# Optimization experiments

Measured on AMD Instinct MI355X. Metric: run time of the kernel, lower is better.

The kernel has to match this reference:

```python
import jax, jax.numpy as jnp
import numpy as np

TOKENS, IN_F, OUT_F = 8192, 4096, 4096
INPUT_ZERO_POINT = 3  # Z_x, baked into shifted_q_bias at quantization time
QMIN, QMAX = -128, 127  # 8-bit signed range


def setup_inputs() -> dict:
    key = jax.random.key(0)
    k1, k2, k3, k4 = jax.random.split(key, 4)
    # int8-valued quantized activations and per-output-channel symmetric int8 weights
    q_x = jax.random.randint(k1, (TOKENS, IN_F), -128, 128, dtype=jnp.int32)
    q_weight = jax.random.randint(k2, (OUT_F, IN_F), -127, 128, dtype=jnp.int32)
    # per-output-channel weight scale (symmetric per-channel quantization)
    weight_scale = jax.random.uniform(k3, (OUT_F,), minval=1e-3, maxval=1e-2, dtype=jnp.float32)
    # int32 quantized bias; shifted by the input zero-point correction term:
    # shifted_q_bias = q_bias - Z_x * q_W.sum(dim=1)
    q_bias = jax.random.randint(k4, (OUT_F,), -(2 ** 15), 2 ** 15, dtype=jnp.int32)
    shifted_q_bias = q_bias - INPUT_ZERO_POINT * jnp.sum(q_weight, axis=1, dtype=jnp.int32)
    return {
        "q_x": q_x,
        "q_weight": q_weight,
        "shifted_q_bias": shifted_q_bias,
        "weight_scale": weight_scale,
        "input_scale": jnp.float32(0.02),
        "output_scale": jnp.float32(0.05),
        "output_zero_point": jnp.float32(-5.0),
    }


def reference(q_x, q_weight, shifted_q_bias, weight_scale, input_scale, output_scale, output_zero_point):
    # GPU path of get_matmul_quantized_output: float-cast int GEMM with fused bias
    acc = jnp.dot(q_x.astype(jnp.float32), q_weight.T.astype(jnp.float32))
    acc = acc + shifted_q_bias.astype(jnp.float32)  # [tokens, out]
    # per-output-channel requant scale: S_W * S_X / S_Y
    scale = weight_scale * input_scale / output_scale  # [out]
    y = scale * acc + output_zero_point
    return jnp.clip(jnp.round(y), QMIN, QMAX).astype(jnp.int8)
```

## Files before the change

kernel.cpp:

```cpp
#include <hip/hip_runtime.h>

#define TOKENS 8192
#define IN_F   4096
#define OUT_F  4096

#define BM 256
#define BN 256
#define BKB 128
#define NT (IN_F / BKB)
#define NI (NT / 2)

using int4v = __attribute__((ext_vector_type(4))) int;
typedef __attribute__((address_space(3))) char       lds_char_t;
typedef const __attribute__((address_space(1))) char glob_char_t;

__global__ void pack_i32_to_i8(const int* __restrict__ src, int* __restrict__ dst, int n4) {
    int stride = gridDim.x * blockDim.x;
    for (int i = blockIdx.x * blockDim.x + threadIdx.x; i < n4; i += stride) {
        int4v v = ((const int4v*)src)[i];
        dst[i] = (v.x & 0xff) | ((v.y & 0xff) << 8) | ((v.z & 0xff) << 16) | (v.w << 24);
    }
}

__global__ __launch_bounds__(512, 2) void qgemm_i8(
    const signed char* __restrict__ A,
    const signed char* __restrict__ Bw,
    const int*   __restrict__ bias,
    const float* __restrict__ wscale,
    const float* __restrict__ p_si, const float* __restrict__ p_so, const float* __restrict__ p_zp,
    int* __restrict__ C)
{
    constexpr int N = OUT_F, K = IN_F;
    constexpr int NBN = N / BN;

    __shared__ __align__(16) signed char smem[131072];

    int nwg = gridDim.x, bid = blockIdx.x, swz = bid;
    if ((nwg & 7) == 0) { int cpx = nwg >> 3; swz = (bid & 7) * cpx + (bid >> 3); }
    int bm = swz / NBN, bn = swz - bm * NBN;

    const int t = threadIdx.x, wid = t >> 6, l = t & 63;
    const int wr = wid >> 2, wc = wid & 3, lr = l & 15, lg = l >> 4;

    const int k0off = ((lg       ^ (lr & 7)) << 4);
    const int k1off = (((4 + lg) ^ (lr & 7)) << 4);
    const int arow = (wr * 128 + lr) * 128;
    const int brow = (wc * 64  + lr) * 128;

    const int srow = t >> 3;
    const int scol = (((t & 7) ^ ((t >> 3) & 7)) << 4);
    const signed char* gApl = A  + (size_t)(bm * BM + srow) * K + scol;
    const signed char* gBpl = Bw + (size_t)(bn * BN + srow) * K + scol;

#define STA(bufOff_, h_, tt_) do {                                                                 \
    __builtin_amdgcn_global_load_lds((glob_char_t*)(gApl + (size_t)((h_)*128      ) * K + (tt_)*BKB), \
        (lds_char_t*)smem + (bufOff_) + (h_)*16384 +        wid*1024, 16, 0, 0);                   \
    __builtin_amdgcn_global_load_lds((glob_char_t*)(gApl + (size_t)((h_)*128 + 64 ) * K + (tt_)*BKB), \
        (lds_char_t*)smem + (bufOff_) + (h_)*16384 + 8192 + wid*1024, 16, 0, 0);                   \
} while (0)
#define STB(bufOff_, h_, tt_) do {                                                                 \
    __builtin_amdgcn_global_load_lds((glob_char_t*)(gBpl + (size_t)((h_)*128      ) * K + (tt_)*BKB), \
        (lds_char_t*)smem + (bufOff_) + 32768 + (h_)*16384 +        wid*1024, 16, 0, 0);           \
    __builtin_amdgcn_global_load_lds((glob_char_t*)(gBpl + (size_t)((h_)*128 + 64 ) * K + (tt_)*BKB), \
        (lds_char_t*)smem + (bufOff_) + 32768 + (h_)*16384 + 8192 + wid*1024, 16, 0, 0);           \
} while (0)

#define LDA4(bufOff_, mb_) do { _Pragma("unroll") for (int mm = 0; mm < 4; ++mm) {                 \
    a[(mb_)+mm][0] = *(const int4v*)(smem + (bufOff_) + arow + ((mb_)+mm)*2048 + k0off);           \
    a[(mb_)+mm][1] = *(const int4v*)(smem + (bufOff_) + arow + ((mb_)+mm)*2048 + k1off); } } while (0)
#define LDB2(bufOff_, nb_) do { _Pragma("unroll") for (int nn = 0; nn < 2; ++nn) {                 \
    b[(nb_)+nn][0] = *(const int4v*)(smem + (bufOff_) + 32768 + brow + ((nb_)+nn)*2048 + k0off);   \
    b[(nb_)+nn][1] = *(const int4v*)(smem + (bufOff_) + 32768 + brow + ((nb_)+nn)*2048 + k1off); } } while (0)

#define MF(mb_, nb_) do { _Pragma("unroll") for (int kk = 0; kk < 2; ++kk)                         \
    _Pragma("unroll") for (int mm = 0; mm < 4; ++mm)                                               \
    _Pragma("unroll") for (int nn = 0; nn < 2; ++nn)                                               \
        acc[(mb_)+mm][(nb_)+nn] = __builtin_amdgcn_mfma_i32_16x16x64_i8(                           \
            a[(mb_)+mm][kk], b[(nb_)+nn][kk], acc[(mb_)+mm][(nb_)+nn], 0, 0, 0); } while (0)

#define SP1 __builtin_amdgcn_s_setprio(1)
#define SP0 __builtin_amdgcn_s_setprio(0)
#define BAR __builtin_amdgcn_s_barrier()
#define VM(n_) asm volatile("s_waitcnt vmcnt(" #n_ ")" ::: "memory")

    int4v acc[8][4] = {};
    int4v a[8][2], b[4][2];

    STA(0, 0, 0); STA(0, 1, 0); STB(0, 0, 0); STB(0, 1, 0);
    STA(65536, 0, 1); STA(65536, 1, 1);
    VM(4);
    BAR;
    LDB2(0, 0); LDA4(0, 0);

#define ITER_FULL(i_) do {                                                                         \
    const int t1 = 2*(i_)+1, t2 = 2*(i_)+2, t3 = 2*(i_)+3;                                         \
     STB(65536, 0, t1); LDA4(0, 4);                  SP1; MF(0, 0); SP0;        BAR;         \
     STB(65536, 1, t1); LDB2(0, 2);                  SP1; MF(4, 0); SP0;        BAR;         \
     STA(0, 0, t2);                                  SP1; MF(0, 2); SP0; VM(2); BAR;         \
     STA(0, 1, t2);     LDB2(65536, 0); LDA4(65536, 0); SP1; MF(4, 2); SP0;     BAR;         \
     STB(0, 0, t2);     LDA4(65536, 4);              SP1; MF(0, 0); SP0;        BAR;         \
     STB(0, 1, t2);     LDB2(65536, 2);              SP1; MF(4, 0); SP0;        BAR;         \
     STA(65536, 0, t3);                              SP1; MF(0, 2); SP0; VM(2); BAR;         \
     STA(65536, 1, t3); LDB2(0, 0); LDA4(0, 0);      SP1; MF(4, 2); SP0;        BAR;         \
} while (0)

#define ITER_TAIL() do {                                                                           \
     STB(65536, 0, 31); LDA4(0, 4);                  SP1; MF(0, 0); SP0;        BAR;         \
     STB(65536, 1, 31); LDB2(0, 2);                  SP1; MF(4, 0); SP0;        BAR;         \
                                                     SP1; MF(0, 2); SP0; VM(0); BAR;         \
     LDB2(65536, 0); LDA4(65536, 0);                 SP1; MF(4, 2); SP0;        BAR;         \
     LDA4(65536, 4);                                 SP1; MF(0, 0); SP0;        BAR;         \
     LDB2(65536, 2);                                 SP1; MF(4, 0); SP0;        BAR;         \
                                                     SP1; MF(0, 2); SP0;        BAR;         \
                                                     SP1; MF(4, 2); SP0;                     \
} while (0)

    for (int i = 0; i < NI - 1; ++i) ITER_FULL(i);
    ITER_TAIL();

#undef ITER_TAIL
#undef ITER_FULL
#undef VM
#undef BAR
#undef SP0
#undef SP1
#undef MF
#undef LDB2
#undef LDA4
#undef STB
#undef STA

    float si = p_si[0], so = p_so[0], z = p_zp[0];
    float rs = si / so;

    #pragma unroll
    for (int n = 0; n < 4; ++n) {
        int col = bn * BN + wc * 64 + n * 16 + lr;
        float sc = wscale[col] * rs;
        int   bs = bias[col];
        #pragma unroll
        for (int m = 0; m < 8; ++m) {
            int row = bm * BM + wr * 128 + m * 16 + lg * 4;
            #pragma unroll
            for (int r = 0; r < 4; ++r) {
                float y = sc * (float)(acc[m][n][r] + bs) + z;
                y = rintf(y);
                y = fminf(fmaxf(y, -128.0f), 127.0f);
                C[(size_t)(row + r) * N + col] = (int)y;
            }
        }
    }
}

__global__ void qgemm_naive(const int* __restrict__ qx, const int* __restrict__ qw,
                            const int* __restrict__ bias, const float* __restrict__ wscale,
                            const float* __restrict__ si, const float* __restrict__ so,
                            const float* __restrict__ zp, int* __restrict__ out) {
    int idx = blockIdx.x * blockDim.x + threadIdx.x;
    if (idx >= TOKENS * OUT_F) return;
    int row = idx / OUT_F, col = idx - row * OUT_F;
    const int4v* xa = (const int4v*)(qx + (size_t)row * IN_F);
    const int4v* wb = (const int4v*)(qw + (size_t)col * IN_F);
    int acc = 0;
    for (int k = 0; k < IN_F / 4; ++k) {
        int4v a = xa[k], b = wb[k];
        acc += a.x * b.x + a.y * b.y + a.z * b.z + a.w * b.w;
    }
    float y = wscale[col] * si[0] / so[0] * (float)(acc + bias[col]) + zp[0];
    y = fminf(fmaxf(rintf(y), -128.0f), 127.0f);
    out[idx] = (int)y;
}

extern "C" void kernel_launch(void* const* d_in, const int* in_sizes, int n_in,
                              void* d_out, int out_size, void* d_ws, size_t ws_size,
                              hipStream_t stream) {
    const int*   q_x    = (const int*)d_in[0];
    const int*   q_w    = (const int*)d_in[1];
    const int*   bias   = (const int*)d_in[2];
    const float* wscale = (const float*)d_in[3];
    const float* s_in   = (const float*)d_in[4];
    const float* s_out  = (const float*)d_in[5];
    const float* zp     = (const float*)d_in[6];
    int* out = (int*)d_out;

    const size_t needA = (size_t)TOKENS * IN_F;
    const size_t needB = (size_t)OUT_F * IN_F;

    if (ws_size >= needA + needB) {
        signed char* pA = (signed char*)d_ws;
        signed char* pB = pA + needA;
        pack_i32_to_i8<<<2048, 256, 0, stream>>>(q_x, (int*)pA, (int)(needA / 4));
        pack_i32_to_i8<<<1024, 256, 0, stream>>>(q_w, (int*)pB, (int)(needB / 4));
        int grid = (TOKENS / BM) * (OUT_F / BN);
        qgemm_i8<<<grid, 512, 0, stream>>>(pA, pB, bias, wscale, s_in, s_out, zp, out);
    } else {
        int total = TOKENS * OUT_F;
        qgemm_naive<<<(total + 255) / 256, 256, 0, stream>>>(q_x, q_w, bias, wscale, s_in, s_out, zp, out);
    }
}
```

Measured before the change: 181.6 us.

## Switch int8 GEMM to 32x32x32 MFMA with inline-asm LDS reads and restructured pipeline

Replaces the 16x16x64 int8 MFMA tiling with 32x32x32 MFMA fragments, so each wave holds a 4x2 grid of 16-element accumulators. LDS reads become inline-asm ds_read_b128 with immediate offsets from precomputed swizzled base pointers that toggle between the two buffers. The main loop is rescheduled into four half-tile phases with ping-pong register fragments, explicit lgkmcnt/vmcnt waits and sched barriers. The aim is fewer MFMA issues, fewer LDS reads per MAC and less address arithmetic. In exchange, waiting on vmcnt(0) at every stage may expose global-load latency, and the epilogue row mapping must match the 32x32 output layout.

New measurement: 199.6 us. 9.9% more time.

```diff
diff --git a/kernel.cpp b/kernel.cpp
--- a/kernel.cpp
+++ b/kernel.cpp
@@ -10,7 +10,8 @@
 #define NT (IN_F / BKB)
 #define NI (NT / 2)
 
-using int4v = __attribute__((ext_vector_type(4))) int;
+using int4v  = __attribute__((ext_vector_type(4)))  int;
+using int16v = __attribute__((ext_vector_type(16))) int;
 typedef __attribute__((address_space(3))) char       lds_char_t;
 typedef const __attribute__((address_space(1))) char glob_char_t;
 
@@ -40,12 +41,17 @@
     int bm = swz / NBN, bn = swz - bm * NBN;
 
     const int t = threadIdx.x, wid = t >> 6, l = t & 63;
-    const int wr = wid >> 2, wc = wid & 3, lr = l & 15, lg = l >> 4;
-
-    const int k0off = ((lg       ^ (lr & 7)) << 4);
-    const int k1off = (((4 + lg) ^ (lr & 7)) << 4);
-    const int arow = (wr * 128 + lr) * 128;
-    const int brow = (wc * 64  + lr) * 128;
+    const int wr = wid >> 2, wc = wid & 3;
+    const int l31 = l & 31, hi = l >> 5, l7 = l & 7;
+
+    const unsigned aB0 = (unsigned)(uintptr_t)((lds_char_t*)smem + (wr * 128 + l31) * 128);
+    const unsigned bB0 = (unsigned)(uintptr_t)((lds_char_t*)smem + 32768 + (wc * 64 + l31) * 128);
+    unsigned aB[4], bB[4];
+    #pragma unroll
+    for (int k = 0; k < 4; ++k) {
+        unsigned x = (unsigned)(((k * 2 + hi) ^ l7) << 4);
+        aB[k] = aB0 + x; bB[k] = bB0 + x;
+    }
 
     const int srow = t >> 3;
     const int scol = (((t & 7) ^ ((t >> 3) & 7)) << 4);
@@ -65,54 +71,69 @@
         (lds_char_t*)smem + (bufOff_) + 32768 + (h_)*16384 + 8192 + wid*1024, 16, 0, 0);           \
 } while (0)
 
-#define LDA4(bufOff_, mb_) do { _Pragma("unroll") for (int mm = 0; mm < 4; ++mm) {                 \
-    a[(mb_)+mm][0] = *(const int4v*)(smem + (bufOff_) + arow + ((mb_)+mm)*2048 + k0off);           \
-    a[(mb_)+mm][1] = *(const int4v*)(smem + (bufOff_) + arow + ((mb_)+mm)*2048 + k1off); } } while (0)
-#define LDB2(bufOff_, nb_) do { _Pragma("unroll") for (int nn = 0; nn < 2; ++nn) {                 \
-    b[(nb_)+nn][0] = *(const int4v*)(smem + (bufOff_) + 32768 + brow + ((nb_)+nn)*2048 + k0off);   \
-    b[(nb_)+nn][1] = *(const int4v*)(smem + (bufOff_) + 32768 + brow + ((nb_)+nn)*2048 + k1off); } } while (0)
-
-#define MF(mb_, nb_) do { _Pragma("unroll") for (int kk = 0; kk < 2; ++kk)                         \
-    _Pragma("unroll") for (int mm = 0; mm < 4; ++mm)                                               \
-    _Pragma("unroll") for (int nn = 0; nn < 2; ++nn)                                               \
-        acc[(mb_)+mm][(nb_)+nn] = __builtin_amdgcn_mfma_i32_16x16x64_i8(                           \
-            a[(mb_)+mm][kk], b[(nb_)+nn][kk], acc[(mb_)+mm][(nb_)+nn], 0, 0, 0); } while (0)
-
+#define DSR(dst_, base_, imm_) \
+    asm volatile("ds_read_b128 %0, %1 offset:" #imm_ : "=&v"(dst_) : "v"(base_))
+
+#define RDH(aF_, bF_, k0_, k1_) do {                                     \
+    DSR(aF_[0][0], aB[k0_], 0);     DSR(aF_[0][1], aB[k1_], 0);          \
+    DSR(aF_[1][0], aB[k0_], 4096);  DSR(aF_[1][1], aB[k1_], 4096);       \
+    DSR(aF_[2][0], aB[k0_], 8192);  DSR(aF_[2][1], aB[k1_], 8192);       \
+    DSR(aF_[3][0], aB[k0_], 12288); DSR(aF_[3][1], aB[k1_], 12288);      \
+    DSR(bF_[0][0], bB[k0_], 0);     DSR(bF_[0][1], bB[k1_], 0);          \
+    DSR(bF_[1][0], bB[k0_], 4096);  DSR(bF_[1][1], bB[k1_], 4096); } while (0)
+
+#define SLOTP() do { _Pragma("unroll") for (int k_ = 0; k_ < 4; ++k_) { aB[k_] += 65536u; bB[k_] += 65536u; } } while (0)
+#define SLOTM() do { _Pragma("unroll") for (int k_ = 0; k_ < 4; ++k_) { aB[k_] -= 65536u; bB[k_] -= 65536u; } } while (0)
+
+#define MF(aF_, bF_) do { _Pragma("unroll") for (int kk = 0; kk < 2; ++kk)                         \
+    _Pragma("unroll") for (int mi = 0; mi < 4; ++mi)                                               \
+    _Pragma("unroll") for (int ni = 0; ni < 2; ++ni)                                               \
+        acc[mi][ni] = __builtin_amdgcn_mfma_i32_32x32x32_i8(                                       \
+            aF_[mi][kk], bF_[ni][kk], acc[mi][ni], 0, 0, 0); } while (0)
+
+#define SCB __builtin_amdgcn_sched_barrier(0)
 #define SP1 __builtin_amdgcn_s_setprio(1)
 #define SP0 __builtin_amdgcn_s_setprio(0)
 #define BAR __builtin_amdgcn_s_barrier()
-#define VM(n_) asm volatile("s_waitcnt vmcnt(" #n_ ")" ::: "memory")
-
-    int4v acc[8][4] = {};
-    int4v a[8][2], b[4][2];
+#define VM0 asm volatile("s_waitcnt vmcnt(0)" ::: "memory")
+#define WK0 do { asm volatile("s_waitcnt lgkmcnt(0)" ::: "memory"); SCB; } while (0)
+
+    int16v acc[4][2] = {};
+    int4v aE[4][2], aO[4][2], bE[2][2], bO[2][2];
 
     STA(0, 0, 0); STA(0, 1, 0); STB(0, 0, 0); STB(0, 1, 0);
     STA(65536, 0, 1); STA(65536, 1, 1);
-    VM(4);
+    VM0;
     BAR;
-    LDB2(0, 0); LDA4(0, 0);
+    RDH(aE, bE, 0, 1);
+    WK0;
 
 #define ITER_FULL(i_) do {                                                                         \
-    const int t1 = 2*(i_)+1, t2 = 2*(i_)+2, t3 = 2*(i_)+3;                                         \
-     STB(65536, 0, t1); LDA4(0, 4);                  SP1; MF(0, 0); SP0;        BAR;         \
-     STB(65536, 1, t1); LDB2(0, 2);                  SP1; MF(4, 0); SP0;        BAR;         \
-     STA(0, 0, t2);                                  SP1; MF(0, 2); SP0; VM(2); BAR;         \
-     STA(0, 1, t2);     LDB2(65536, 0); LDA4(65536, 0); SP1; MF(4, 2); SP0;     BAR;         \
-     STB(0, 0, t2);     LDA4(65536, 4);              SP1; MF(0, 0); SP0;        BAR;         \
-     STB(0, 1, t2);     LDB2(65536, 2);              SP1; MF(4, 0); SP0;        BAR;         \
-     STA(65536, 0, t3);                              SP1; MF(0, 2); SP0; VM(2); BAR;         \
-     STA(65536, 1, t3); LDB2(0, 0); LDA4(0, 0);      SP1; MF(4, 2); SP0;        BAR;         \
+    const int u1 = 2*(i_) + 1, u2 = 2*(i_) + 2, u3 = 2*(i_) + 3;                                   \
+                     \
+    STB(65536, 0, u1); STB(65536, 1, u1);                                                          \
+    RDH(aO, bO, 2, 3); SCB; SP1; MF(aE, bE); SP0; SCB; WK0; VM0; SLOTP(); BAR;                     \
+                 \
+    STA(0, 0, u2); STA(0, 1, u2);                                                                  \
+    RDH(aE, bE, 0, 1); SCB; SP1; MF(aO, bO); SP0; SCB; WK0; BAR;                                   \
+             \
+    STB(0, 0, u2); STB(0, 1, u2);                                                                  \
+    RDH(aO, bO, 2, 3); SCB; SP1; MF(aE, bE); SP0; SCB; WK0; VM0; SLOTM(); BAR;                     \
+                       \
+    STA(65536, 0, u3); STA(65536, 1, u3);                                                          \
+    RDH(aE, bE, 0, 1); SCB; SP1; MF(aO, bO); SP0; SCB; WK0; BAR;                                   \
 } while (0)
 
 #define ITER_TAIL() do {                                                                           \
-     STB(65536, 0, 31); LDA4(0, 4);                  SP1; MF(0, 0); SP0;        BAR;         \
-     STB(65536, 1, 31); LDB2(0, 2);                  SP1; MF(4, 0); SP0;        BAR;         \
-                                                     SP1; MF(0, 2); SP0; VM(0); BAR;         \
-     LDB2(65536, 0); LDA4(65536, 0);                 SP1; MF(4, 2); SP0;        BAR;         \
-     LDA4(65536, 4);                                 SP1; MF(0, 0); SP0;        BAR;         \
-     LDB2(65536, 2);                                 SP1; MF(4, 0); SP0;        BAR;         \
-                                                     SP1; MF(0, 2); SP0;        BAR;         \
-                                                     SP1; MF(4, 2); SP0;                     \
+                                \
+    STB(65536, 0, 31); STB(65536, 1, 31);                                                          \
+    RDH(aO, bO, 2, 3); SCB; SP1; MF(aE, bE); SP0; SCB; WK0; VM0; SLOTP(); BAR;                     \
+                       \
+    RDH(aE, bE, 0, 1); SCB; SP1; MF(aO, bO); SP0; SCB; WK0; BAR;                                   \
+                                                                   \
+    RDH(aO, bO, 2, 3); SCB; SP1; MF(aE, bE); SP0; SCB; WK0;                                        \
+                                                                                \
+    SP1; MF(aO, bO); SP0;                                                                          \
 } while (0)
 
     for (int i = 0; i < NI - 1; ++i) ITER_FULL(i);
@@ -120,13 +141,17 @@
 
 #undef ITER_TAIL
 #undef ITER_FULL
-#undef VM
+#undef WK0
+#undef VM0
 #undef BAR
 #undef SP0
 #undef SP1
+#undef SCB
 #undef MF
-#undef LDB2
-#undef LDA4
+#undef SLOTM
+#undef SLOTP
+#undef RDH
+#undef DSR
 #undef STB
 #undef STA
 
@@ -134,19 +159,20 @@
     float rs = si / so;
 
     #pragma unroll
-    for (int n = 0; n < 4; ++n) {
-        int col = bn * BN + wc * 64 + n * 16 + lr;
+    for (int ni = 0; ni < 2; ++ni) {
+        int col = bn * BN + wc * 64 + ni * 32 + l31;
         float sc = wscale[col] * rs;
         int   bs = bias[col];
         #pragma unroll
-        for (int m = 0; m < 8; ++m) {
-            int row = bm * BM + wr * 128 + m * 16 + lg * 4;
+        for (int mi = 0; mi < 4; ++mi) {
+            int rowb = bm * BM + wr * 128 + mi * 32 + 4 * hi;
             #pragma unroll
-            for (int r = 0; r < 4; ++r) {
-                float y = sc * (float)(acc[m][n][r] + bs) + z;
+            for (int r = 0; r < 16; ++r) {
+                int row = rowb + (r & 3) + 8 * (r >> 2);
+                float y = sc * (float)(acc[mi][ni][r] + bs) + z;
                 y = rintf(y);
                 y = fminf(fmaxf(y, -128.0f), 127.0f);
-                C[(size_t)(row + r) * N + col] = (int)y;
+                C[(size_t)row * N + col] = (int)y;
             }
         }
     }
```
